# Optimization experiments

Measured on AMD Instinct MI355X. Metric: run time of the kernel, lower is better.

The kernel has to match this reference:

```python
import jax, jax.numpy as jnp
import numpy as np

B, S, D, H = 2, 2048, 1024, 16
HD = D // H

def setup_inputs() -> dict:
    key = jax.random.key(0)
    ks = jax.random.split(key, 5)
    scale = 1.0 / np.sqrt(D)
    x = jax.random.normal(ks[0], (B, S, D), dtype=jnp.float32)
    W_qkv = jax.random.normal(ks[1], (D, 3 * D), dtype=jnp.float32) * scale
    b_qkv = jnp.zeros((3 * D,), dtype=jnp.float32)
    W_proj = jax.random.normal(ks[2], (D, D), dtype=jnp.float32) * scale
    b_proj = jnp.zeros((D,), dtype=jnp.float32)
    return {"x": x, "W_qkv": W_qkv, "b_qkv": b_qkv, "W_proj": W_proj, "b_proj": b_proj}

def reference(x, W_qkv, b_qkv, W_proj, b_proj):
    # qkv projection: [B,S,3D]
    qkv = jnp.einsum('bsd,df->bsf', x, W_qkv) + b_qkv
    q, k, v = jnp.split(qkv, 3, axis=-1)
    # reshape to heads: [B,H,S,hd]
    q = q.reshape(B, S, H, HD).transpose(0, 2, 1, 3)
    k = k.reshape(B, S, H, HD).transpose(0, 2, 1, 3)
    v = v.reshape(B, S, H, HD).transpose(0, 2, 1, 3)
    scores = jnp.einsum('bhqd,bhkd->bhqk', q, k) / jnp.sqrt(jnp.float32(HD))
    attn = jax.nn.softmax(scores, axis=-1)
    out = jnp.einsum('bhqk,bhkd->bhqd', attn, v)
    out = out.transpose(0, 2, 1, 3).reshape(B, S, D)
    return jnp.einsum('bsd,df->bsf', out, W_proj) + b_proj
```

## Files before the change

kernel.cpp:

```cpp
#include <hip/hip_runtime.h>

#define BATCH 2
#define SLEN 2048
#define DMODEL 1024
#define NHEAD 16
#define HDIM 64
#define MROWS (BATCH * SLEN)

typedef __attribute__((ext_vector_type(8))) short bf16x8;
typedef __attribute__((ext_vector_type(4))) short bf16x4;
typedef __attribute__((ext_vector_type(4))) float f32x4;
typedef __attribute__((ext_vector_type(8))) _Float16 f16x8;
typedef __attribute__((ext_vector_type(4))) _Float16 f16x4;

__device__ inline short f2bf(float x) {
    union { float f; unsigned u; } v; v.f = x;
    unsigned r = (v.u + 0x7FFFu + ((v.u >> 16) & 1u)) >> 16;
    return (short)r;
}
__device__ inline float bf2f(short h) {
    union { unsigned u; float f; } v; v.u = ((unsigned)(unsigned short)h) << 16;
    return v.f;
}
__device__ inline unsigned fbits(float x) {
    union { float f; unsigned u; } v; v.f = x; return v.u;
}
__device__ inline float hw_exp2(float x) {
    float r;
    asm("v_exp_f32 %0, %1" : "=v"(r) : "v"(x));
    return r;
}

__global__ __launch_bounds__(256) void cast_f16(
    const float* __restrict__ in, _Float16* __restrict__ out, int n4)
{
    int i = blockIdx.x * 256 + threadIdx.x;
    if (i >= n4) return;
    float4 f = ((const float4*)in)[i];
    f16x4 h;
    h[0] = (_Float16)f.x; h[1] = (_Float16)f.y;
    h[2] = (_Float16)f.z; h[3] = (_Float16)f.w;
    ((f16x4*)out)[i] = h;
}

__global__ __launch_bounds__(256) void transpose_f16(
    const float* __restrict__ in, _Float16* __restrict__ outT, int K, int N)
{
    __shared__ float T[64][68];
    const int tid = threadIdx.x;
    const int n0 = blockIdx.x * 64, k0 = blockIdx.y * 64;
#pragma unroll
    for (int i = 0; i < 4; i++) {
        int idx = tid + i * 256;
        int r = idx >> 4, c4 = idx & 15;
        *(float4*)&T[r][c4 * 4] = *(const float4*)&in[(size_t)(k0 + r) * N + n0 + c4 * 4];
    }
    __syncthreads();
#pragma unroll
    for (int i = 0; i < 4; i++) {
        int idx = tid + i * 256;
        int n = idx >> 4, kg = idx & 15;
        f16x4 h;
#pragma unroll
        for (int j = 0; j < 4; j++)
            h[j] = (_Float16)T[kg * 4 + j][n];
        *(f16x4*)&outT[(size_t)(n0 + n) * K + k0 + kg * 4] = h;
    }
}

__global__ __launch_bounds__(256) void transpose_v(
    const short* __restrict__ qkv, short* __restrict__ vT)
{
    __shared__ short T[64 * 68];
    const int tid = threadIdx.x;
    const int bid = blockIdx.x;
    const int st = bid & 31, h = (bid >> 5) & 15, b = bid >> 9;
    const int s0 = st * 64;
    const short* src = qkv + (size_t)b * SLEN * (3 * DMODEL) + 2 * DMODEL + h * HDIM;

    const int srow = tid >> 3, sc8 = tid & 7;
#pragma unroll
    for (int it = 0; it < 2; it++) {
        int s = srow + it * 32;
        *(bf16x8*)&T[s * 68 + sc8 * 8] =
            *(const bf16x8*)&src[(size_t)(s0 + s) * (3 * DMODEL) + sc8 * 8];
    }
    __syncthreads();

    const int d = tid >> 2, sq = tid & 3;
    short* dst = vT + ((size_t)(b * NHEAD + h) * HDIM + d) * SLEN + s0 + sq * 16;
    bf16x8 o0, o1;
#pragma unroll
    for (int j = 0; j < 8; j++) {
        o0[j] = T[(sq * 16 + j) * 68 + d];
        o1[j] = T[(sq * 16 + 8 + j) * 68 + d];
    }
    *(bf16x8*)&dst[0] = o0;
    *(bf16x8*)&dst[8] = o1;
}

#define GSTR 40

template<int OUT_BF16>
__global__ __launch_bounds__(256) void gemm_f16(
    const _Float16* __restrict__ A, const _Float16* __restrict__ Bw,
    const float* __restrict__ bias, void* __restrict__ Cout,
    int M, int N, int K)
{
    __shared__ _Float16 As[128 * GSTR], Bs[128 * GSTR];

    const int tid  = threadIdx.x;
    const int wave = tid >> 6, lane = tid & 63;
    const int quad = lane >> 4, lr = lane & 15;
    const int wm = (wave >> 1) * 64, wn = (wave & 1) * 64;
    const int row0 = blockIdx.y * 128, col0 = blockIdx.x * 128;

    f32x4 acc[4][4];
#pragma unroll
    for (int i = 0; i < 4; i++)
#pragma unroll
        for (int j = 0; j < 4; j++) acc[i][j] = (f32x4){0.f, 0.f, 0.f, 0.f};

    const int sr = tid >> 2, sc = tid & 3;

    const _Float16* ap0 = A  + (size_t)(row0 + sr) * K + sc * 8;
    const _Float16* ap1 = ap0 + (size_t)64 * K;
    const _Float16* bp0 = Bw + (size_t)(col0 + sr) * K + sc * 8;
    const _Float16* bp1 = bp0 + (size_t)64 * K;

    f16x8 apre[2], bpre[2];
    apre[0] = *(const f16x8*)ap0; apre[1] = *(const f16x8*)ap1;
    bpre[0] = *(const f16x8*)bp0; bpre[1] = *(const f16x8*)bp1;
    ap0 += 32; ap1 += 32; bp0 += 32; bp1 += 32;

    const int ls = sr * GSTR + sc * 8;

    for (int k0 = 0; k0 < K; k0 += 32) {
        *(f16x8*)&As[ls] = apre[0];
        *(f16x8*)&As[ls + 64 * GSTR] = apre[1];
        *(f16x8*)&Bs[ls] = bpre[0];
        *(f16x8*)&Bs[ls + 64 * GSTR] = bpre[1];

        if (k0 + 32 < K) {
            apre[0] = *(const f16x8*)ap0; apre[1] = *(const f16x8*)ap1;
            bpre[0] = *(const f16x8*)bp0; bpre[1] = *(const f16x8*)bp1;
            ap0 += 32; ap1 += 32; bp0 += 32; bp1 += 32;
        }

        __syncthreads();

        f16x8 af[4];
#pragma unroll
        for (int mt = 0; mt < 4; mt++)
            af[mt] = *(const f16x8*)&As[(wm + mt * 16 + lr) * GSTR + quad * 8];
#pragma unroll
        for (int nt = 0; nt < 4; nt++) {
            f16x8 b = *(const f16x8*)&Bs[(wn + nt * 16 + lr) * GSTR + quad * 8];
#pragma unroll
            for (int mt = 0; mt < 4; mt++)
                acc[mt][nt] = __builtin_amdgcn_mfma_f32_16x16x32_f16(af[mt], b, acc[mt][nt], 0, 0, 0);
        }

        __syncthreads();
    }

#pragma unroll
    for (int mt = 0; mt < 4; mt++) {
#pragma unroll
        for (int nt = 0; nt < 4; nt++) {
            int col = col0 + wn + nt * 16 + lr;
            float bv = bias[col];
#pragma unroll
            for (int r = 0; r < 4; r++) {
                int row = row0 + wm + mt * 16 + quad * 4 + r;
                float v = acc[mt][nt][r] + bv;
                if (OUT_BF16)
                    ((short*)Cout)[(size_t)row * N + col] = f2bf(v);
                else
                    ((float*)Cout)[(size_t)row * N + col] = v;
            }
        }
    }
}

#define ASTR 72
#define NT   (SLEN / 64)
#define QK_SCALE_LOG2E 0.1803368801111244f

__global__ __launch_bounds__(256) void attn_mfma(
    const short* __restrict__ qkv, const short* __restrict__ vT,
    _Float16* __restrict__ attn)
{
    __shared__ short Ks[2][64 * ASTR];
    __shared__ short Vt[2][64 * ASTR];

    const int tid  = threadIdx.x;
    const int lane = tid & 63;
    const int wave = tid >> 6;
    const int quad = lane >> 4;
    const int lr   = lane & 15;
    const int wq0  = wave * 16;

    const int bid = blockIdx.x;
    const int qt = bid & 31;
    const int h  = (bid >> 5) & 15;
    const int b  = bid >> 9;
    const int q0 = qt * 64;

    const short* qbase = qkv + (size_t)b * SLEN * (3 * DMODEL) + h * HDIM;
    const short* kbase = qbase + DMODEL;
    const short* vtbase = vT + (size_t)(b * NHEAD + h) * HDIM * SLEN;

    bf16x8 qf[2];
#pragma unroll
    for (int ds2 = 0; ds2 < 2; ds2++) {
        bf16x8 q = *(const bf16x8*)&qbase[(size_t)(q0 + wq0 + lr) * (3 * DMODEL) + ds2 * 32 + quad * 8];
#pragma unroll
        for (int j = 0; j < 8; j++)
            q[j] = f2bf(bf2f(q[j]) * QK_SCALE_LOG2E);
        qf[ds2] = q;
    }

    bf16x4 ones;
#pragma unroll
    for (int j = 0; j < 4; j++) ones[j] = (short)0x3F80;

    f32x4 oacc[4];
#pragma unroll
    for (int t = 0; t < 4; t++) oacc[t] = (f32x4){0.f, 0.f, 0.f, 0.f};
    f32x4 sacc = {0.f, 0.f, 0.f, 0.f};

    const int srow = tid >> 3, sc8 = tid & 7;

    const short* kp0 = kbase + (size_t)srow * (3 * DMODEL) + sc8 * 8;
    const short* kp1 = kp0 + 32 * (3 * DMODEL);
    const short* vp0 = vtbase + (size_t)srow * SLEN + sc8 * 8;
    const short* vp1 = vp0 + 32 * SLEN;

    bf16x8 kpre[2], vpre[2];
    kpre[0] = *(const bf16x8*)kp0; kpre[1] = *(const bf16x8*)kp1;
    vpre[0] = *(const bf16x8*)vp0; vpre[1] = *(const bf16x8*)vp1;
    kp0 += 64 * (3 * DMODEL); kp1 += 64 * (3 * DMODEL);
    vp0 += 64; vp1 += 64;

    for (int kt = 0; kt < NT; kt++) {
        const int cur = kt & 1;
        short* ks = Ks[cur];
        short* vt = Vt[cur];

        *(bf16x8*)&ks[srow * ASTR + sc8 * 8] = kpre[0];
        *(bf16x8*)&ks[(srow + 32) * ASTR + sc8 * 8] = kpre[1];
        *(bf16x8*)&vt[srow * ASTR + sc8 * 8] = vpre[0];
        *(bf16x8*)&vt[(srow + 32) * ASTR + sc8 * 8] = vpre[1];

        if (kt + 1 < NT) {
            kpre[0] = *(const bf16x8*)kp0; kpre[1] = *(const bf16x8*)kp1;
            vpre[0] = *(const bf16x8*)vp0; vpre[1] = *(const bf16x8*)vp1;
            kp0 += 64 * (3 * DMODEL); kp1 += 64 * (3 * DMODEL);
            vp0 += 64; vp1 += 64;
        }

        __syncthreads();

#pragma unroll
        for (int ct = 0; ct < 4; ct++) {
            bf16x8 kf0 = *(const bf16x8*)&ks[(ct * 16 + lr) * ASTR + quad * 8];
            bf16x8 kf1 = *(const bf16x8*)&ks[(ct * 16 + lr) * ASTR + 32 + quad * 8];

            f32x4 st = {0.f, 0.f, 0.f, 0.f};
            st = __builtin_amdgcn_mfma_f32_16x16x32_bf16(kf0, qf[0], st, 0, 0, 0);
            st = __builtin_amdgcn_mfma_f32_16x16x32_bf16(kf1, qf[1], st, 0, 0, 0);

            float p0[4];
#pragma unroll
            for (int r = 0; r < 4; r++) p0[r] = hw_exp2(st[r]);
            union { uint2 u; bf16x4 v; } pk0;
            pk0.u.x = __builtin_amdgcn_perm(fbits(p0[1]), fbits(p0[0]), 0x07060302u);
            pk0.u.y = __builtin_amdgcn_perm(fbits(p0[3]), fbits(p0[2]), 0x07060302u);
            bf16x4 pf0 = pk0.v;

            sacc = __builtin_amdgcn_mfma_f32_16x16x16bf16_1k(ones, pf0, sacc, 0, 0, 0);
#pragma unroll
            for (int dt = 0; dt < 4; dt++) {
                bf16x4 vf = *(const bf16x4*)&vt[(dt * 16 + lr) * ASTR + ct * 16 + quad * 4];
                oacc[dt] = __builtin_amdgcn_mfma_f32_16x16x16bf16_1k(vf, pf0, oacc[dt], 0, 0, 0);
            }
        }
    }

    {
        const float inv = 1.0f / sacc[0];
        const int row = b * SLEN + q0 + wq0 + lr;
#pragma unroll
        for (int dt = 0; dt < 4; dt++) {
            f16x4 h4;
#pragma unroll
            for (int r = 0; r < 4; r++)
                h4[r] = (_Float16)(oacc[dt][r] * inv);
            int col = h * HDIM + dt * 16 + quad * 4;
            *(f16x4*)&attn[(size_t)row * DMODEL + col] = h4;
        }
    }
}

extern "C" void kernel_launch(void* const* d_in, const int* in_sizes, int n_in,
                              void* d_out, int out_size, void* d_ws, size_t ws_size,
                              hipStream_t stream) {
    (void)in_sizes; (void)n_in; (void)out_size; (void)ws_size;
    const float* x     = (const float*)d_in[0];
    const float* Wqkv  = (const float*)d_in[1];
    const float* bqkv  = (const float*)d_in[2];
    const float* Wproj = (const float*)d_in[3];
    const float* bproj = (const float*)d_in[4];
    float* out = (float*)d_out;

    short* qkv = (short*)d_ws;
    _Float16* xf = (_Float16*)(qkv + (size_t)MROWS * 3 * DMODEL);
    _Float16* wq = xf + (size_t)MROWS * DMODEL;
    _Float16* wp = wq + (size_t)3 * DMODEL * DMODEL;
    short* vT = (short*)(wp + (size_t)DMODEL * DMODEL);
    _Float16* attnb = (_Float16*)(vT + (size_t)MROWS * DMODEL);

    cast_f16<<<dim3(MROWS * DMODEL / 4 / 256), 256, 0, stream>>>(x, xf, MROWS * DMODEL / 4);
    transpose_f16<<<dim3(3 * DMODEL / 64, DMODEL / 64), 256, 0, stream>>>(Wqkv, wq, DMODEL, 3 * DMODEL);
    transpose_f16<<<dim3(DMODEL / 64, DMODEL / 64), 256, 0, stream>>>(Wproj, wp, DMODEL, DMODEL);

    gemm_f16<1><<<dim3(3 * DMODEL / 128, MROWS / 128), 256, 0, stream>>>(
        xf, wq, bqkv, (void*)qkv, MROWS, 3 * DMODEL, DMODEL);

    transpose_v<<<dim3(BATCH * NHEAD * (SLEN / 64)), 256, 0, stream>>>(qkv, vT);

    attn_mfma<<<dim3(BATCH * NHEAD * (SLEN / 64)), 256, 0, stream>>>(qkv, vT, attnb);

    gemm_f16<0><<<dim3(DMODEL / 128, MROWS / 128), 256, 0, stream>>>(
        attnb, wp, bproj, (void*)out, MROWS, DMODEL, DMODEL);
}
```

Baseline: 209.4 us.

## Split attention key tiles across wave pairs, each covering two query subtiles

Each wave now handles 32 query rows (two 16-row subtiles) over half of the key columns in every tile, instead of 16 query rows over all columns. K and V fragments read from LDS are reused across both query subtiles, which halves LDS fragment traffic per MFMA. Partial output and row sums from the two column-half waves are reduced through shared memory at the end. This costs more accumulator registers and extra synchronization in the epilogue.

```diff
diff --git a/kernel.cpp b/kernel.cpp
--- a/kernel.cpp
+++ b/kernel.cpp
@@ -185,21 +185,24 @@
 
 #define ASTR 72
 #define NT   (SLEN / 64)
+#define RSTR 20
 #define QK_SCALE_LOG2E 0.1803368801111244f
 
 __global__ __launch_bounds__(256) void attn_mfma(
     const short* __restrict__ qkv, const short* __restrict__ vT,
     _Float16* __restrict__ attn)
 {
-    __shared__ short Ks[2][64 * ASTR];
-    __shared__ short Vt[2][64 * ASTR];
+    __shared__ __align__(16) char smem[2 * 64 * ASTR * 2 * 2];
+    short* KsBuf = (short*)smem;
+    short* VtBuf = KsBuf + 2 * 64 * ASTR;
 
     const int tid  = threadIdx.x;
     const int lane = tid & 63;
     const int wave = tid >> 6;
     const int quad = lane >> 4;
     const int lr   = lane & 15;
-    const int wq0  = wave * 16;
+    const int qhalf  = wave >> 1;
+    const int cthalf = wave & 1;
 
     const int bid = blockIdx.x;
     const int qt = bid & 31;
@@ -211,24 +214,28 @@
     const short* kbase = qbase + DMODEL;
     const short* vtbase = vT + (size_t)(b * NHEAD + h) * HDIM * SLEN;
 
-    bf16x8 qf[2];
-#pragma unroll
-    for (int ds2 = 0; ds2 < 2; ds2++) {
-        bf16x8 q = *(const bf16x8*)&qbase[(size_t)(q0 + wq0 + lr) * (3 * DMODEL) + ds2 * 32 + quad * 8];
-#pragma unroll
-        for (int j = 0; j < 8; j++)
-            q[j] = f2bf(bf2f(q[j]) * QK_SCALE_LOG2E);
-        qf[ds2] = q;
-    }
+    bf16x8 qf[2][2];
+#pragma unroll
+    for (int qs = 0; qs < 2; qs++)
+#pragma unroll
+        for (int ds2 = 0; ds2 < 2; ds2++) {
+            bf16x8 q = *(const bf16x8*)&qbase[(size_t)(q0 + qhalf * 32 + qs * 16 + lr) * (3 * DMODEL) + ds2 * 32 + quad * 8];
+#pragma unroll
+            for (int j = 0; j < 8; j++)
+                q[j] = f2bf(bf2f(q[j]) * QK_SCALE_LOG2E);
+            qf[qs][ds2] = q;
+        }
 
     bf16x4 ones;
 #pragma unroll
     for (int j = 0; j < 4; j++) ones[j] = (short)0x3F80;
 
-    f32x4 oacc[4];
-#pragma unroll
-    for (int t = 0; t < 4; t++) oacc[t] = (f32x4){0.f, 0.f, 0.f, 0.f};
-    f32x4 sacc = {0.f, 0.f, 0.f, 0.f};
+    f32x4 oacc[2][4];
+#pragma unroll
+    for (int qs = 0; qs < 2; qs++)
+#pragma unroll
+        for (int t = 0; t < 4; t++) oacc[qs][t] = (f32x4){0.f, 0.f, 0.f, 0.f};
+    f32x4 sacc[2] = {{0.f, 0.f, 0.f, 0.f}, {0.f, 0.f, 0.f, 0.f}};
 
     const int srow = tid >> 3, sc8 = tid & 7;
 
@@ -245,8 +252,8 @@
 
     for (int kt = 0; kt < NT; kt++) {
         const int cur = kt & 1;
-        short* ks = Ks[cur];
-        short* vt = Vt[cur];
+        short* ks = KsBuf + cur * 64 * ASTR;
+        short* vt = VtBuf + cur * 64 * ASTR;
 
         *(bf16x8*)&ks[srow * ASTR + sc8 * 8] = kpre[0];
         *(bf16x8*)&ks[(srow + 32) * ASTR + sc8 * 8] = kpre[1];
@@ -263,43 +270,99 @@
         __syncthreads();
 
 #pragma unroll
-        for (int ct = 0; ct < 4; ct++) {
+        for (int ct2 = 0; ct2 < 2; ct2++) {
+            const int ct = cthalf * 2 + ct2;
             bf16x8 kf0 = *(const bf16x8*)&ks[(ct * 16 + lr) * ASTR + quad * 8];
             bf16x8 kf1 = *(const bf16x8*)&ks[(ct * 16 + lr) * ASTR + 32 + quad * 8];
-
-            f32x4 st = {0.f, 0.f, 0.f, 0.f};
-            st = __builtin_amdgcn_mfma_f32_16x16x32_bf16(kf0, qf[0], st, 0, 0, 0);
-            st = __builtin_amdgcn_mfma_f32_16x16x32_bf16(kf1, qf[1], st, 0, 0, 0);
-
-            float p0[4];
-#pragma unroll
-            for (int r = 0; r < 4; r++) p0[r] = hw_exp2(st[r]);
-            union { uint2 u; bf16x4 v; } pk0;
-            pk0.u.x = __builtin_amdgcn_perm(fbits(p0[1]), fbits(p0[0]), 0x07060302u);
-            pk0.u.y = __builtin_amdgcn_perm(fbits(p0[3]), fbits(p0[2]), 0x07060302u);
-            bf16x4 pf0 = pk0.v;
-
-            sacc = __builtin_amdgcn_mfma_f32_16x16x16bf16_1k(ones, pf0, sacc, 0, 0, 0);
-#pragma unroll
-            for (int dt = 0; dt < 4; dt++) {
-                bf16x4 vf = *(const bf16x4*)&vt[(dt * 16 + lr) * ASTR + ct * 16 + quad * 4];
-                oacc[dt] = __builtin_amdgcn_mfma_f32_16x16x16bf16_1k(vf, pf0, oacc[dt], 0, 0, 0);
+            bf16x4 vf0 = *(const bf16x4*)&vt[(0 * 16 + lr) * ASTR + ct * 16 + quad * 4];
+            bf16x4 vf1 = *(const bf16x4*)&vt[(1 * 16 + lr) * ASTR + ct * 16 + quad * 4];
+            bf16x4 vf2 = *(const bf16x4*)&vt[(2 * 16 + lr) * ASTR + ct * 16 + quad * 4];
+            bf16x4 vf3 = *(const bf16x4*)&vt[(3 * 16 + lr) * ASTR + ct * 16 + quad * 4];
+
+#pragma unroll
+            for (int qs = 0; qs < 2; qs++) {
+                f32x4 st = {0.f, 0.f, 0.f, 0.f};
+                st = __builtin_amdgcn_mfma_f32_16x16x32_bf16(kf0, qf[qs][0], st, 0, 0, 0);
+                st = __builtin_amdgcn_mfma_f32_16x16x32_bf16(kf1, qf[qs][1], st, 0, 0, 0);
+
+                float p0[4];
+#pragma unroll
+                for (int r = 0; r < 4; r++) p0[r] = hw_exp2(st[r]);
+                union { uint2 u; bf16x4 v; } pk0;
+                pk0.u.x = __builtin_amdgcn_perm(fbits(p0[1]), fbits(p0[0]), 0x07060302u);
+                pk0.u.y = __builtin_amdgcn_perm(fbits(p0[3]), fbits(p0[2]), 0x07060302u);
+                bf16x4 pf0 = pk0.v;
+
+                sacc[qs] = __builtin_amdgcn_mfma_f32_16x16x16bf16_1k(ones, pf0, sacc[qs], 0, 0, 0);
+                oacc[qs][0] = __builtin_amdgcn_mfma_f32_16x16x16bf16_1k(vf0, pf0, oacc[qs][0], 0, 0, 0);
+                oacc[qs][1] = __builtin_amdgcn_mfma_f32_16x16x16bf16_1k(vf1, pf0, oacc[qs][1], 0, 0, 0);
+                oacc[qs][2] = __builtin_amdgcn_mfma_f32_16x16x16bf16_1k(vf2, pf0, oacc[qs][2], 0, 0, 0);
+                oacc[qs][3] = __builtin_amdgcn_mfma_f32_16x16x16bf16_1k(vf3, pf0, oacc[qs][3], 0, 0, 0);
             }
         }
     }
 
-    {
-        const float inv = 1.0f / sacc[0];
-        const int row = b * SLEN + q0 + wq0 + lr;
-#pragma unroll
-        for (int dt = 0; dt < 4; dt++) {
-            f16x4 h4;
-#pragma unroll
-            for (int r = 0; r < 4; r++)
-                h4[r] = (_Float16)(oacc[dt][r] * inv);
-            int col = h * HDIM + dt * 16 + quad * 4;
-            *(f16x4*)&attn[(size_t)row * DMODEL + col] = h4;
-        }
+    __syncthreads();
+    float* Lf = (float*)smem;
+    float* myrow = Lf + (wave * 64 + lane) * RSTR;
+
+    if (cthalf == 1) {
+        *(f32x4*)&myrow[0]  = oacc[0][0];
+        *(f32x4*)&myrow[4]  = oacc[0][1];
+        *(f32x4*)&myrow[8]  = oacc[0][2];
+        *(f32x4*)&myrow[12] = oacc[0][3];
+        myrow[16] = sacc[0][0];
+    }
+    __syncthreads();
+    if (cthalf == 0) {
+        const float* pr = Lf + ((wave ^ 1) * 64 + lane) * RSTR;
+        f32x4 o0 = oacc[0][0] + *(const f32x4*)&pr[0];
+        f32x4 o1 = oacc[0][1] + *(const f32x4*)&pr[4];
+        f32x4 o2 = oacc[0][2] + *(const f32x4*)&pr[8];
+        f32x4 o3 = oacc[0][3] + *(const f32x4*)&pr[12];
+        const float inv = 1.0f / (sacc[0][0] + pr[16]);
+        const int row = b * SLEN + q0 + qhalf * 32 + lr;
+        f16x4 h4;
+#pragma unroll
+        for (int r = 0; r < 4; r++) h4[r] = (_Float16)(o0[r] * inv);
+        *(f16x4*)&attn[(size_t)row * DMODEL + h * HDIM + 0 * 16 + quad * 4] = h4;
+#pragma unroll
+        for (int r = 0; r < 4; r++) h4[r] = (_Float16)(o1[r] * inv);
+        *(f16x4*)&attn[(size_t)row * DMODEL + h * HDIM + 1 * 16 + quad * 4] = h4;
+#pragma unroll
+        for (int r = 0; r < 4; r++) h4[r] = (_Float16)(o2[r] * inv);
+        *(f16x4*)&attn[(size_t)row * DMODEL + h * HDIM + 2 * 16 + quad * 4] = h4;
+#pragma unroll
+        for (int r = 0; r < 4; r++) h4[r] = (_Float16)(o3[r] * inv);
+        *(f16x4*)&attn[(size_t)row * DMODEL + h * HDIM + 3 * 16 + quad * 4] = h4;
+        *(f32x4*)&myrow[0]  = oacc[1][0];
+        *(f32x4*)&myrow[4]  = oacc[1][1];
+        *(f32x4*)&myrow[8]  = oacc[1][2];
+        *(f32x4*)&myrow[12] = oacc[1][3];
+        myrow[16] = sacc[1][0];
+    }
+    __syncthreads();
+    if (cthalf == 1) {
+        const float* pr = Lf + ((wave ^ 1) * 64 + lane) * RSTR;
+        f32x4 o0 = oacc[1][0] + *(const f32x4*)&pr[0];
+        f32x4 o1 = oacc[1][1] + *(const f32x4*)&pr[4];
+        f32x4 o2 = oacc[1][2] + *(const f32x4*)&pr[8];
+        f32x4 o3 = oacc[1][3] + *(const f32x4*)&pr[12];
+        const float inv = 1.0f / (sacc[1][0] + pr[16]);
+        const int row = b * SLEN + q0 + qhalf * 32 + 16 + lr;
+        f16x4 h4;
+#pragma unroll
+        for (int r = 0; r < 4; r++) h4[r] = (_Float16)(o0[r] * inv);
+        *(f16x4*)&attn[(size_t)row * DMODEL + h * HDIM + 0 * 16 + quad * 4] = h4;
+#pragma unroll
+        for (int r = 0; r < 4; r++) h4[r] = (_Float16)(o1[r] * inv);
+        *(f16x4*)&attn[(size_t)row * DMODEL + h * HDIM + 1 * 16 + quad * 4] = h4;
+#pragma unroll
+        for (int r = 0; r < 4; r++) h4[r] = (_Float16)(o2[r] * inv);
+        *(f16x4*)&attn[(size_t)row * DMODEL + h * HDIM + 2 * 16 + quad * 4] = h4;
+#pragma unroll
+        for (int r = 0; r < 4; r++) h4[r] = (_Float16)(o3[r] * inv);
+        *(f16x4*)&attn[(size_t)row * DMODEL + h * HDIM + 3 * 16 + quad * 4] = h4;
     }
 }
 
```

Measured after the change: 206.2 us. About the same (-1.5%).
